# Kernel optimization log

Measured on AMD Instinct MI355X. Metric: run time of the kernel, lower is better.

Reference implementation:

```python
import jax, jax.numpy as jnp
import numpy as np

B, N, K = 16, 2048, 16          # clouds, points per cloud, knn k
C_IN, C_OUT = 64, 64

def setup_inputs() -> dict:
    key = jax.random.key(0)
    ks = jax.random.split(key, 8)
    s_in = 1.0 / np.sqrt(C_IN)
    return {
        "x": jax.random.normal(ks[0], (B * N, C_IN), jnp.float32),
        "pos": jax.random.normal(ks[1], (B * N, 3), jnp.float32),
        "batch": jnp.repeat(jnp.arange(B, dtype=jnp.int32), N),
        "W_pos": jax.random.normal(ks[2], (3, C_OUT), jnp.float32) / np.sqrt(3.0),
        "b_pos": jnp.zeros((C_OUT,), jnp.float32),
        "W_attn": jax.random.normal(ks[3], (C_OUT, C_OUT), jnp.float32) / np.sqrt(C_OUT),
        "b_attn": jnp.zeros((C_OUT,), jnp.float32),
        "W_val": jax.random.normal(ks[4], (C_IN, C_OUT), jnp.float32) * s_in,
        "W_src": jax.random.normal(ks[5], (C_IN, C_OUT), jnp.float32) * s_in,
        "W_dst": jax.random.normal(ks[6], (C_IN, C_OUT), jnp.float32) * s_in,
    }

def _gather(a, idx):
    # a: [B, N, D], idx: [B, N, K+1] -> [B, N, K+1, D]
    return jax.vmap(lambda ab, ib: ab[ib])(a, idx)

def reference(x, pos, batch, W_pos, b_pos, W_attn, b_attn, W_val, W_src, W_dst):
    # batch is assumed contiguous with equal-size clouds (B clouds of N points),
    # so batch-restricted knn_graph == per-cloud knn after reshape.
    posr = pos.reshape(B, N, 3)
    xr = x.reshape(B, N, C_IN)
    # knn_graph(loop=False): exclude self, then PointTransformerConv re-adds self loops
    d2 = jnp.sum((posr[:, :, None, :] - posr[:, None, :, :]) ** 2, axis=-1)  # [B,N,N]
    d2 = d2 + jnp.eye(N, dtype=d2.dtype) * 1e10
    _, nbr = jax.lax.top_k(-d2, K)                                # [B,N,K] sources j per target i
    self_idx = jnp.broadcast_to(jnp.arange(N)[None, :, None], (B, N, 1))
    nbr = jnp.concatenate([nbr, self_idx], axis=2)                # self loop -> [B,N,K+1]
    alpha_i = xr @ W_dst                                          # lin_dst(x_i)  [B,N,C_OUT]
    alpha_j = _gather(xr @ W_src, nbr)                            # lin_src(x_j)  [B,N,K+1,C_OUT]
    val_j = _gather(xr @ W_val, nbr)                              # lin(x_j)
    pos_j = _gather(posr, nbr)                                    # [B,N,K+1,3]
    delta = (posr[:, :, None, :] - pos_j) @ W_pos + b_pos         # pos_nn(pos_i - pos_j)
    alpha = alpha_i[:, :, None, :] - alpha_j + delta              # subtraction attention
    alpha = alpha @ W_attn + b_attn                               # attn_nn
    alpha = jax.nn.softmax(alpha, axis=2)                         # segment softmax per target i
    out = jnp.sum(alpha * (val_j + delta), axis=2)                # weighted scatter-sum
    return out.reshape(B * N, C_OUT)
```

## Files before the change

### kernel.cpp

```cpp
#include <hip/hip_runtime.h>
#include <math.h>

#define BBATCH 16
#define NPC    2048
#define KNBR   16
#define NPTS   (BBATCH*NPC)
#define NGEMM  512
#define NKNN   512
#define BUFCAP 512

__global__ __launch_bounds__(1024) void fused_gk_kernel(
    const float* __restrict__ pos, const float* __restrict__ x,
    const float* __restrict__ Wpos, const float* __restrict__ bpos,
    const float* __restrict__ Wattn, const float* __restrict__ battn,
    const float* __restrict__ Wval, const float* __restrict__ Wsrc,
    const float* __restrict__ Wdst,
    int* __restrict__ nbr, float* __restrict__ A2, float* __restrict__ S2,
    float* __restrict__ V, float* __restrict__ WP2, float* __restrict__ bb) {
  __shared__ __align__(16) char smem[65536];
  int t = threadIdx.x;
  int bid = blockIdx.x;
  int c = t & 63, g = t >> 6;

  if (bid == NGEMM + NKNN) {
    if (t < 64) {
      for (int r = 0; r < 3; ++r) {
        float a = 0.f;
        for (int d = 0; d < 64; ++d) a += Wpos[r * 64 + d] * Wattn[d * 64 + t];
        WP2[r * 64 + t] = a;
      }
      float a = battn[t];
      for (int d = 0; d < 64; ++d) a += bpos[d] * Wattn[d * 64 + t];
      bb[t] = a;
    }
    return;
  }

  if (bid < NGEMM) {
    float* R0 = (float*)smem;
    float* R1 = (float*)(smem + 16384);
    float* R2 = (float*)(smem + 32768);
    float* R3 = (float*)(smem + 49152);
    float4* R04 = (float4*)R0;
    float4* R34 = (float4*)R3;

    R34[t] = ((const float4*)Wattn)[t];
    R04[t] = ((const float4*)Wdst)[t];
    __syncthreads();
    {
      float a0 = 0, a1 = 0, a2 = 0, a3 = 0;
      for (int k = 0; k < 64; ++k) {
        float w = R3[k * 64 + c];
        a0 += R0[(g * 4 + 0) * 64 + k] * w;
        a1 += R0[(g * 4 + 1) * 64 + k] * w;
        a2 += R0[(g * 4 + 2) * 64 + k] * w;
        a3 += R0[(g * 4 + 3) * 64 + k] * w;
      }
      R1[(g * 4 + 0) * 64 + c] = a0; R1[(g * 4 + 1) * 64 + c] = a1;
      R1[(g * 4 + 2) * 64 + c] = a2; R1[(g * 4 + 3) * 64 + c] = a3;
    }
    __syncthreads();
    R04[t] = ((const float4*)Wsrc)[t];
    __syncthreads();
    {
      float a0 = 0, a1 = 0, a2 = 0, a3 = 0;
      for (int k = 0; k < 64; ++k) {
        float w = R3[k * 64 + c];
        a0 += R0[(g * 4 + 0) * 64 + k] * w;
        a1 += R0[(g * 4 + 1) * 64 + k] * w;
        a2 += R0[(g * 4 + 2) * 64 + k] * w;
        a3 += R0[(g * 4 + 3) * 64 + k] * w;
      }
      R2[(g * 4 + 0) * 64 + c] = a0; R2[(g * 4 + 1) * 64 + c] = a1;
      R2[(g * 4 + 2) * 64 + c] = a2; R2[(g * 4 + 3) * 64 + c] = a3;
    }
    __syncthreads();
    R34[t] = ((const float4*)Wval)[t];
    R04[t] = ((const float4*)(x + (size_t)bid * 64 * 64))[t];
    __syncthreads();

    float v0 = 0, v1 = 0, v2 = 0, v3 = 0;
    float a0 = 0, a1 = 0, a2 = 0, a3 = 0;
    float s0 = 0, s1 = 0, s2 = 0, s3 = 0;
    const float4* xr0 = (const float4*)(R0 + (g * 4 + 0) * 64);
    const float4* xr1 = (const float4*)(R0 + (g * 4 + 1) * 64);
    const float4* xr2 = (const float4*)(R0 + (g * 4 + 2) * 64);
    const float4* xr3 = (const float4*)(R0 + (g * 4 + 3) * 64);
#pragma unroll 4
    for (int k4 = 0; k4 < 16; ++k4) {
      float4 q0 = xr0[k4], q1 = xr1[k4], q2 = xr2[k4], q3 = xr3[k4];
#pragma unroll
      for (int kk = 0; kk < 4; ++kk) {
        int k = k4 * 4 + kk;
        float wv = R3[k * 64 + c];
        float wa = R1[k * 64 + c];
        float ws = R2[k * 64 + c];
        float e0 = (kk == 0) ? q0.x : (kk == 1) ? q0.y : (kk == 2) ? q0.z : q0.w;
        float e1 = (kk == 0) ? q1.x : (kk == 1) ? q1.y : (kk == 2) ? q1.z : q1.w;
        float e2 = (kk == 0) ? q2.x : (kk == 1) ? q2.y : (kk == 2) ? q2.z : q2.w;
        float e3 = (kk == 0) ? q3.x : (kk == 1) ? q3.y : (kk == 2) ? q3.z : q3.w;
        v0 += e0 * wv; v1 += e1 * wv; v2 += e2 * wv; v3 += e3 * wv;
        a0 += e0 * wa; a1 += e1 * wa; a2 += e2 * wa; a3 += e3 * wa;
        s0 += e0 * ws; s1 += e1 * ws; s2 += e2 * ws; s3 += e3 * ws;
      }
    }
    size_t o0 = ((size_t)bid * 64 + g * 4 + 0) * 64 + c;
    V[o0] = v0; A2[o0] = a0; S2[o0] = s0;
    size_t o1 = o0 + 64;  V[o1] = v1; A2[o1] = a1; S2[o1] = s1;
    size_t o2 = o0 + 128; V[o2] = v2; A2[o2] = a2; S2[o2] = s2;
    size_t o3 = o0 + 192; V[o3] = v3; A2[o3] = a3; S2[o3] = s3;
    return;
  }

  int kb = bid - NGEMM;
  float4* pos4 = (float4*)smem;
  unsigned short* buf = (unsigned short*)(smem + 32768);
  int cloud = kb >> 5;
  const float* pc = pos + (size_t)cloud * NPC * 3;
  for (int p = t; p < NPC; p += 1024)
    pos4[p] = make_float4(pc[3 * p], pc[3 * p + 1], pc[3 * p + 2], 0.f);
  __syncthreads();

  int w = g, lane = c;
  for (int u = 0; u < 4; ++u) {
    int lt = u * 16 + w;
    int gi = kb * 64 + lt;
    int ti = gi & (NPC - 1);
    float4 tp = pos4[ti];
    float tx = tp.x, ty = tp.y, tz = tp.z;

    int bkt[32];
#pragma unroll
    for (int cc = 0; cc < 32; ++cc) {
      int j = cc * 64 + lane;
      float4 q = pos4[j];
      float dx = tx - q.x, dy = ty - q.y, dz = tz - q.z;
      float d2 = dx * dx + dy * dy + dz * dz;
      int b = (int)(__float_as_uint(d2) >> 20) - 896;
      bkt[cc] = max(0, min(255, b));
    }

    int lo = 0, hi = 255;
    for (int it = 0; it < 8; ++it) {
      int mid = (lo + hi) >> 1;
      int cnt = 0;
#pragma unroll
      for (int cc = 0; cc < 32; ++cc)
        cnt += (int)__popcll(__ballot(bkt[cc] <= mid));
      if (cnt >= 17) hi = mid; else lo = mid + 1;
    }
    int Tp1 = min(hi + 1, 255);

    int base = 0;
#pragma unroll
    for (int cc = 0; cc < 32; ++cc) {
      bool f = (bkt[cc] <= Tp1);
      unsigned long long mm = __ballot(f);
      unsigned int pre = __builtin_amdgcn_mbcnt_hi(
          (unsigned)(mm >> 32), __builtin_amdgcn_mbcnt_lo((unsigned)mm, 0u));
      if (f) {
        int p = base + (int)pre;
        if (p < BUFCAP) buf[w * BUFCAP + p] = (unsigned short)(cc * 64 + lane);
      }
      base += (int)__popcll(mm);
    }
    int n = min(base, BUFCAP);
    double txd = (double)tx, tyd = (double)ty, tzd = (double)tz;

    if (n <= 64) {
      unsigned long long gb = 0xFFFFFFFFFFFFFFFFull;
      int gj = 0x40000000 + lane;
      if (lane < n) {
        int j = buf[w * BUFCAP + lane];
        if (j != ti) {
          float4 q = pos4[j];
          double dx = __dsub_rn(txd, (double)q.x);
          double dy = __dsub_rn(tyd, (double)q.y);
          double dz = __dsub_rn(tzd, (double)q.z);
          double d2 = __dadd_rn(__dadd_rn(__dmul_rn(dx, dx), __dmul_rn(dy, dy)),
                                __dmul_rn(dz, dz));
          gb = (unsigned long long)__double_as_longlong(d2);
          gj = j;
        }
      }
      for (int k = 2; k <= 64; k <<= 1) {
        for (int jj = k >> 1; jj > 0; jj >>= 1) {
          unsigned long long ob = __shfl_xor(gb, jj);
          int oj = __shfl_xor(gj, jj);
          bool keepmin = (((lane & k) == 0) == ((lane & jj) == 0));
          bool less = (ob < gb) || (ob == gb && oj < gj);
          if (keepmin == less) { gb = ob; gj = oj; }
        }
      }
      if (lane < KNBR) nbr[(size_t)gi * KNBR + lane] = gj;
    } else {
      unsigned long long kb2[8];
      int id2[8];
#pragma unroll
      for (int r = 0; r < 8; ++r) {
        int e = r * 64 + lane;
        kb2[r] = 0xFFFFFFFFFFFFFFFFull;
        id2[r] = 0x40000000 + e;
        if (e < n) {
          int j = buf[w * BUFCAP + e];
          if (j != ti) {
            float4 q = pos4[j];
            double dx = __dsub_rn(txd, (double)q.x);
            double dy = __dsub_rn(tyd, (double)q.y);
            double dz = __dsub_rn(tzd, (double)q.z);
            double d2 = __dadd_rn(
                __dadd_rn(__dmul_rn(dx, dx), __dmul_rn(dy, dy)),
                __dmul_rn(dz, dz));
            kb2[r] = (unsigned long long)__double_as_longlong(d2);
            id2[r] = j;
          }
        }
      }
      for (int r = 0; r < KNBR; ++r) {
        unsigned long long lb = kb2[0];
        int lj = id2[0];
#pragma unroll
        for (int cc = 1; cc < 8; ++cc)
          if (kb2[cc] < lb || (kb2[cc] == lb && id2[cc] < lj)) {
            lb = kb2[cc]; lj = id2[cc];
          }
        unsigned long long gb2 = lb;
        int gj2 = lj;
#pragma unroll
        for (int d = 32; d >= 1; d >>= 1) {
          unsigned long long ob = __shfl_xor(gb2, d);
          int oj = __shfl_xor(gj2, d);
          if (ob < gb2 || (ob == gb2 && oj < gj2)) { gb2 = ob; gj2 = oj; }
        }
#pragma unroll
        for (int cc = 0; cc < 8; ++cc)
          if (id2[cc] == gj2) kb2[cc] = 0xFFFFFFFFFFFFFFFFull;
        if (lane == 0) nbr[(size_t)gi * KNBR + r] = gj2;
      }
    }
  }
}

__global__ __launch_bounds__(256) void edge_kernel(
    const float* __restrict__ pos, const int* __restrict__ nbr,
    const float* __restrict__ A2, const float* __restrict__ S2,
    const float* __restrict__ V, const float* __restrict__ WP2,
    const float* __restrict__ bbv, const float* __restrict__ Wpos,
    const float* __restrict__ bpos, float* __restrict__ out) {
  int t = threadIdx.x, w = t >> 6, c = t & 63;
  int gi = blockIdx.x * 4 + w;
  int cloudbase = gi & ~(NPC - 1);
  float pix = pos[(size_t)gi * 3], piy = pos[(size_t)gi * 3 + 1],
        piz = pos[(size_t)gi * 3 + 2];
  float a2 = A2[(size_t)gi * 64 + c];
  float wp0 = WP2[c], wp1 = WP2[64 + c], wp2 = WP2[128 + c], bbc = bbv[c];
  float u0 = Wpos[c], u1 = Wpos[64 + c], u2 = Wpos[128 + c], bpc = bpos[c];

  float lg[17], vl[17];
#pragma unroll
  for (int e = 0; e < 17; ++e) {
    int j = (e < 16) ? nbr[(size_t)gi * KNBR + e] : (gi & (NPC - 1));
    int jg = cloudbase + j;
    float dx = pix - pos[(size_t)jg * 3];
    float dy = piy - pos[(size_t)jg * 3 + 1];
    float dz = piz - pos[(size_t)jg * 3 + 2];
    float s2 = S2[(size_t)jg * 64 + c];
    float v = V[(size_t)jg * 64 + c];
    lg[e] = a2 - s2 + dx * wp0 + dy * wp1 + dz * wp2 + bbc;
    vl[e] = v + dx * u0 + dy * u1 + dz * u2 + bpc;
  }
  float mx = lg[0];
#pragma unroll
  for (int e = 1; e < 17; ++e) mx = fmaxf(mx, lg[e]);
  float den = 0.f, acc = 0.f;
#pragma unroll
  for (int e = 0; e < 17; ++e) {
    float wgt = __expf(lg[e] - mx);
    den += wgt;
    acc += wgt * vl[e];
  }
  out[(size_t)gi * 64 + c] = acc / den;
}

extern "C" void kernel_launch(void* const* d_in, const int* in_sizes, int n_in,
                              void* d_out, int out_size, void* d_ws, size_t ws_size,
                              hipStream_t stream) {
  const float* x     = (const float*)d_in[0];
  const float* pos   = (const float*)d_in[1];
  const float* Wpos  = (const float*)d_in[3];
  const float* bpos  = (const float*)d_in[4];
  const float* Wattn = (const float*)d_in[5];
  const float* battn = (const float*)d_in[6];
  const float* Wval  = (const float*)d_in[7];
  const float* Wsrc  = (const float*)d_in[8];
  const float* Wdst  = (const float*)d_in[9];

  float* ws  = (float*)d_ws;
  float* A2  = ws;
  float* S2  = A2 + (size_t)NPTS * 64;
  float* V   = S2 + (size_t)NPTS * 64;
  float* WP2 = V + (size_t)NPTS * 64;
  float* bb  = WP2 + 192;
  int*   nbr = (int*)(bb + 64);
  float* out = (float*)d_out;

  fused_gk_kernel<<<NGEMM + NKNN + 1, 1024, 0, stream>>>(
      pos, x, Wpos, bpos, Wattn, battn, Wval, Wsrc, Wdst,
      nbr, A2, S2, V, WP2, bb);
  edge_kernel<<<NPTS / 4, 256, 0, stream>>>(pos, nbr, A2, S2, V, WP2, bb,
                                            Wpos, bpos, out);
}
```

Measured before the change: 224.0 us.

## Fuse GEMM, kNN and edge softmax into one persistent kernel with grid barrier

```diff
diff --git a/kernel.cpp b/kernel.cpp
--- a/kernel.cpp
+++ b/kernel.cpp
@@ -5,38 +5,24 @@
 #define NPC    2048
 #define KNBR   16
 #define NPTS   (BBATCH*NPC)
-#define NGEMM  512
-#define NKNN   512
+#define NBLK   512
 #define BUFCAP 512
 
-__global__ __launch_bounds__(1024) void fused_gk_kernel(
+__global__ __launch_bounds__(1024, 8) void mega_kernel(
     const float* __restrict__ pos, const float* __restrict__ x,
     const float* __restrict__ Wpos, const float* __restrict__ bpos,
     const float* __restrict__ Wattn, const float* __restrict__ battn,
     const float* __restrict__ Wval, const float* __restrict__ Wsrc,
     const float* __restrict__ Wdst,
-    int* __restrict__ nbr, float* __restrict__ A2, float* __restrict__ S2,
-    float* __restrict__ V, float* __restrict__ WP2, float* __restrict__ bb) {
+    float* __restrict__ A2, float* __restrict__ S2, float* __restrict__ V,
+    float* __restrict__ WP2, float* __restrict__ bb,
+    unsigned int* __restrict__ bar, float* __restrict__ out) {
   __shared__ __align__(16) char smem[65536];
   int t = threadIdx.x;
   int bid = blockIdx.x;
   int c = t & 63, g = t >> 6;
 
-  if (bid == NGEMM + NKNN) {
-    if (t < 64) {
-      for (int r = 0; r < 3; ++r) {
-        float a = 0.f;
-        for (int d = 0; d < 64; ++d) a += Wpos[r * 64 + d] * Wattn[d * 64 + t];
-        WP2[r * 64 + t] = a;
-      }
-      float a = battn[t];
-      for (int d = 0; d < 64; ++d) a += bpos[d] * Wattn[d * 64 + t];
-      bb[t] = a;
-    }
-    return;
-  }
-
-  if (bid < NGEMM) {
+  {
     float* R0 = (float*)smem;
     float* R1 = (float*)(smem + 16384);
     float* R2 = (float*)(smem + 32768);
@@ -109,13 +95,24 @@
     size_t o1 = o0 + 64;  V[o1] = v1; A2[o1] = a1; S2[o1] = s1;
     size_t o2 = o0 + 128; V[o2] = v2; A2[o2] = a2; S2[o2] = s2;
     size_t o3 = o0 + 192; V[o3] = v3; A2[o3] = a3; S2[o3] = s3;
-    return;
+
+    if (bid == 0 && t < 64) {
+      for (int r = 0; r < 3; ++r) {
+        float a = 0.f;
+        for (int d = 0; d < 64; ++d) a += Wpos[r * 64 + d] * Wattn[d * 64 + t];
+        WP2[r * 64 + t] = a;
+      }
+      float a = battn[t];
+      for (int d = 0; d < 64; ++d) a += bpos[d] * Wattn[d * 64 + t];
+      bb[t] = a;
+    }
   }
-
-  int kb = bid - NGEMM;
+  __syncthreads();
+
   float4* pos4 = (float4*)smem;
   unsigned short* buf = (unsigned short*)(smem + 32768);
-  int cloud = kb >> 5;
+  unsigned short* nbrl = (unsigned short*)(smem + 49152);
+  int cloud = bid >> 5;
   const float* pc = pos + (size_t)cloud * NPC * 3;
   for (int p = t; p < NPC; p += 1024)
     pos4[p] = make_float4(pc[3 * p], pc[3 * p + 1], pc[3 * p + 2], 0.f);
@@ -124,7 +121,7 @@
   int w = g, lane = c;
   for (int u = 0; u < 4; ++u) {
     int lt = u * 16 + w;
-    int gi = kb * 64 + lt;
+    int gi = bid * 64 + lt;
     int ti = gi & (NPC - 1);
     float4 tp = pos4[ti];
     float tx = tp.x, ty = tp.y, tz = tp.z;
@@ -192,7 +189,7 @@
           if (keepmin == less) { gb = ob; gj = oj; }
         }
       }
-      if (lane < KNBR) nbr[(size_t)gi * KNBR + lane] = gj;
+      if (lane < KNBR) nbrl[lt * KNBR + lane] = (unsigned short)gj;
     } else {
       unsigned long long kb2[8];
       int id2[8];
@@ -235,51 +232,59 @@
 #pragma unroll
         for (int cc = 0; cc < 8; ++cc)
           if (id2[cc] == gj2) kb2[cc] = 0xFFFFFFFFFFFFFFFFull;
-        if (lane == 0) nbr[(size_t)gi * KNBR + r] = gj2;
+        if (lane == 0) nbrl[lt * KNBR + r] = (unsigned short)gj2;
       }
     }
   }
-}
-
-__global__ __launch_bounds__(256) void edge_kernel(
-    const float* __restrict__ pos, const int* __restrict__ nbr,
-    const float* __restrict__ A2, const float* __restrict__ S2,
-    const float* __restrict__ V, const float* __restrict__ WP2,
-    const float* __restrict__ bbv, const float* __restrict__ Wpos,
-    const float* __restrict__ bpos, float* __restrict__ out) {
-  int t = threadIdx.x, w = t >> 6, c = t & 63;
-  int gi = blockIdx.x * 4 + w;
-  int cloudbase = gi & ~(NPC - 1);
-  float pix = pos[(size_t)gi * 3], piy = pos[(size_t)gi * 3 + 1],
-        piz = pos[(size_t)gi * 3 + 2];
-  float a2 = A2[(size_t)gi * 64 + c];
-  float wp0 = WP2[c], wp1 = WP2[64 + c], wp2 = WP2[128 + c], bbc = bbv[c];
-  float u0 = Wpos[c], u1 = Wpos[64 + c], u2 = Wpos[128 + c], bpc = bpos[c];
-
-  float lg[17], vl[17];
-#pragma unroll
-  for (int e = 0; e < 17; ++e) {
-    int j = (e < 16) ? nbr[(size_t)gi * KNBR + e] : (gi & (NPC - 1));
-    int jg = cloudbase + j;
-    float dx = pix - pos[(size_t)jg * 3];
-    float dy = piy - pos[(size_t)jg * 3 + 1];
-    float dz = piz - pos[(size_t)jg * 3 + 2];
-    float s2 = S2[(size_t)jg * 64 + c];
-    float v = V[(size_t)jg * 64 + c];
-    lg[e] = a2 - s2 + dx * wp0 + dy * wp1 + dz * wp2 + bbc;
-    vl[e] = v + dx * u0 + dy * u1 + dz * u2 + bpc;
+
+  __threadfence();
+  __syncthreads();
+  if (t == 0) {
+    __atomic_fetch_add(bar, 1u, __ATOMIC_ACQ_REL);
+    while (__hip_atomic_load(bar, __ATOMIC_ACQUIRE,
+                             __HIP_MEMORY_SCOPE_AGENT) < NBLK) {
+      __builtin_amdgcn_s_sleep(8);
+    }
   }
-  float mx = lg[0];
-#pragma unroll
-  for (int e = 1; e < 17; ++e) mx = fmaxf(mx, lg[e]);
-  float den = 0.f, acc = 0.f;
-#pragma unroll
-  for (int e = 0; e < 17; ++e) {
-    float wgt = __expf(lg[e] - mx);
-    den += wgt;
-    acc += wgt * vl[e];
+  __syncthreads();
+  __threadfence();
+
+  {
+    float wp0 = WP2[c], wp1 = WP2[64 + c], wp2 = WP2[128 + c], bbc = bb[c];
+    float u0 = Wpos[c], u1 = Wpos[64 + c], u2 = Wpos[128 + c], bpc = bpos[c];
+    int cloudbase = cloud * NPC;
+    for (int r = 0; r < 4; ++r) {
+      int lt = w * 4 + r;
+      int gi = bid * 64 + lt;
+      int ti = gi & (NPC - 1);
+      float4 pi = pos4[ti];
+      float a2v = A2[(size_t)gi * 64 + c];
+
+      float lg[17], vl[17];
+#pragma unroll
+      for (int e = 0; e < 17; ++e) {
+        int j = (e < 16) ? (int)nbrl[lt * KNBR + e] : ti;
+        float4 q = pos4[j];
+        int jg = cloudbase + j;
+        float dx = pi.x - q.x, dy = pi.y - q.y, dz = pi.z - q.z;
+        float s2 = S2[(size_t)jg * 64 + c];
+        float v = V[(size_t)jg * 64 + c];
+        lg[e] = a2v - s2 + dx * wp0 + dy * wp1 + dz * wp2 + bbc;
+        vl[e] = v + dx * u0 + dy * u1 + dz * u2 + bpc;
+      }
+      float mx = lg[0];
+#pragma unroll
+      for (int e = 1; e < 17; ++e) mx = fmaxf(mx, lg[e]);
+      float den = 0.f, acc = 0.f;
+#pragma unroll
+      for (int e = 0; e < 17; ++e) {
+        float wgt = __expf(lg[e] - mx);
+        den += wgt;
+        acc += wgt * vl[e];
+      }
+      out[(size_t)gi * 64 + c] = acc / den;
+    }
   }
-  out[(size_t)gi * 64 + c] = acc / den;
 }
 
 extern "C" void kernel_launch(void* const* d_in, const int* in_sizes, int n_in,
@@ -301,12 +306,11 @@
   float* V   = S2 + (size_t)NPTS * 64;
   float* WP2 = V + (size_t)NPTS * 64;
   float* bb  = WP2 + 192;
-  int*   nbr = (int*)(bb + 64);
+  unsigned int* bar = (unsigned int*)(bb + 64);
   float* out = (float*)d_out;
 
-  fused_gk_kernel<<<NGEMM + NKNN + 1, 1024, 0, stream>>>(
+  hipMemsetAsync((void*)bar, 0, 64, stream);
+  mega_kernel<<<NBLK, 1024, 0, stream>>>(
       pos, x, Wpos, bpos, Wattn, battn, Wval, Wsrc, Wdst,
-      nbr, A2, S2, V, WP2, bb);
-  edge_kernel<<<NPTS / 4, 256, 0, stream>>>(pos, nbr, A2, S2, V, WP2, bb,
-                                            Wpos, bpos, out);
+      A2, S2, V, WP2, bb, bar, out);
 }
```

Measured after the change: 582.2 us. 2.6x slower.
